# Optimization experiments

Measured on AMD Instinct MI355X. Metric: run time of the kernel, lower is better.

Reference implementation:

```python
import jax, jax.numpy as jnp
from jax import lax
import numpy as np

N, M, P, K = 2, 16384, 5023, 4
C_PLANE, HP = 32, 256
OUT_DIM = 32


def _harmonic(x):
    # pytorch3d HarmonicEmbedding(n=4, logspace, omega_0=1, append_input=True)
    f = jnp.asarray([1.0, 2.0, 4.0, 8.0], x.dtype)
    e = (x[..., None] * f).reshape(x.shape[:-1] + (-1,))  # [..., 12]
    return jnp.concatenate([jnp.sin(e), jnp.cos(e), x], axis=-1)  # [..., 27]


def _grid_sample2d(img, grid):
    # img [C,H,W], grid [M,2] (x->W, y->H) in [-1,1]; bilinear, zero pad, align_corners=False
    C, H, W = img.shape
    x = (grid[:, 0] + 1.0) * (W / 2.0) - 0.5
    y = (grid[:, 1] + 1.0) * (H / 2.0) - 0.5
    x0 = jnp.floor(x); y0 = jnp.floor(y)
    x1 = x0 + 1.0; y1 = y0 + 1.0
    wx1 = x - x0; wx0 = 1.0 - wx1
    wy1 = y - y0; wy0 = 1.0 - wy1
    def gather(ix, iy):
        valid = ((ix >= 0) & (ix < W) & (iy >= 0) & (iy < H)).astype(img.dtype)
        ixc = jnp.clip(ix, 0, W - 1).astype(jnp.int32)
        iyc = jnp.clip(iy, 0, H - 1).astype(jnp.int32)
        return img[:, iyc, ixc] * valid[None, :]  # [C,M]
    out = (gather(x0, y0) * (wx0 * wy0) + gather(x1, y0) * (wx1 * wy0)
           + gather(x0, y1) * (wx0 * wy1) + gather(x1, y1) * (wx1 * wy1))
    return out.T  # [M,C]


def _forward(coordinates, directions, points_position, tex_tplanes, emb_table,
             pw1, pb1, pw2, pb2, fw1, fb1, fw2, fb2, fw3, fb3, dw, db, rw1, rb1, rw2, rb2):
    c = coordinates
    p = points_position
    # --- triplane sampling (EG3D projections (x,y),(x,z),(z,x)), mean over planes ---
    proj = jnp.stack([c[..., :2],
                      c[..., jnp.array([0, 2])],
                      c[..., jnp.array([2, 0])]], axis=1)  # [N,3,M,2]
    tex = jax.vmap(jax.vmap(_grid_sample2d))(tex_tplanes, proj).mean(axis=1)  # [N,M,32]
    # --- KNN (squared distances, ascending, as pytorch3d knn_points) ---
    d2 = (jnp.sum(c * c, -1)[:, :, None] + jnp.sum(p * p, -1)[:, None, :]
          - 2.0 * jnp.einsum('nmc,npc->nmp', c, p))  # [N,M,P]
    negd, idx = lax.top_k(-d2, K)
    dist = -negd  # [N,M,K]
    nn = jax.vmap(lambda pts, i: pts[i])(p, idx)  # [N,M,K,3]
    pf = emb_table[idx]  # [N,M,K,32]
    rel = c[:, :, None, :] - nn
    rel = rel / jnp.maximum(jnp.linalg.norm(rel, axis=-1, keepdims=True), 1e-12)
    h = jnp.concatenate([pf, _harmonic(rel)], axis=-1)  # [N,M,K,59]
    h = jax.nn.relu(h @ pw1 + pb1) @ pw2 + pb2  # [N,M,K,32]
    w = 1.0 / dist
    w = w / jnp.sum(w, axis=1, keepdims=True)  # dim=1 exactly as in source
    pts_feat = jnp.sum(h * w[..., None], axis=2)  # [N,M,32]
    # --- dense MLP stack ---
    feat = jnp.concatenate([tex, pts_feat], axis=-1)  # [N,M,64]
    feat = jax.nn.relu(feat @ fw1 + fb1)
    feat = jax.nn.relu(feat @ fw2 + fb2)
    feat = feat @ fw3 + fb3  # [N,M,128]
    selector = jnp.all((c > -1.0) & (c < 1.0), axis=-1)  # [N,M]
    raw = (jax.nn.softplus(10.0 * (feat @ dw + db)) / 10.0) * selector[..., None]
    densities = 1.0 - jnp.exp(-raw)
    rays = directions / jnp.maximum(jnp.linalg.norm(directions, axis=-1, keepdims=True), 1e-12)
    rgb = jnp.concatenate([feat, _harmonic(rays)], axis=-1)  # [N,M,155]
    rgb = jax.nn.relu(rgb @ rw1 + rb1) @ rw2 + rb2  # [N,M,OUT_DIM]
    rgb = jnp.concatenate([jax.nn.sigmoid(rgb[..., :3]) * (1.0 + 2 * 0.001) - 0.001,
                           rgb[..., 3:]], axis=-1)
    return densities, rgb, dist


def setup_inputs() -> dict:
    key = jax.random.key(0)
    ks = jax.random.split(key, 16)
    rn = lambda k, s, sc=1.0: jax.random.normal(k, s, jnp.float32) * sc
    def lin(k, i, o):
        k1, k2 = jax.random.split(k)
        return rn(k1, (i, o), 1.0 / np.sqrt(i)), rn(k2, (o,), 0.01)
    coordinates = jax.random.uniform(ks[0], (N, M, 3), jnp.float32)
    directions = rn(ks[1], (N, M, 3))
    points_position = jax.random.uniform(ks[2], (N, P, 3), jnp.float32)
    tex_tplanes = rn(ks[3], (N, 3, C_PLANE, HP, HP))
    emb_table = rn(ks[4], (P, 32), 0.02)
    pw1, pb1 = lin(ks[5], 32 + 27, 64)
    pw2, pb2 = lin(ks[6], 64, 32)
    fw1, fb1 = lin(ks[7], 64, 128)
    fw2, fb2 = lin(ks[8], 128, 128)
    fw3, fb3 = lin(ks[9], 128, 128)
    dw, db = lin(ks[10], 128, 1)
    rw1, rb1 = lin(ks[11], 128 + 27, 64)
    rw2, rb2 = lin(ks[12], 64, OUT_DIM)
    return dict(coordinates=coordinates, directions=directions, points_position=points_position,
                tex_tplanes=tex_tplanes, emb_table=emb_table, pw1=pw1, pb1=pb1, pw2=pw2, pb2=pb2,
                fw1=fw1, fb1=fb1, fw2=fw2, fb2=fb2, fw3=fw3, fb3=fb3, dw=dw, db=db,
                rw1=rw1, rb1=rb1, rw2=rw2, rb2=rb2)


def reference(coordinates, directions, points_position, tex_tplanes, emb_table,
              pw1, pb1, pw2, pb2, fw1, fb1, fw2, fb2, fw3, fb3, dw, db, rw1, rb1, rw2, rb2):
    return _forward(coordinates, directions, points_position, tex_tplanes, emb_table,
                    pw1, pb1, pw2, pb2, fw1, fb1, fw2, fb2, fw3, fb3, dw, db, rw1, rb1, rw2, rb2)
```

## Files before the change

kernel.cpp:

```cpp
#include <hip/hip_runtime.h>
#include <float.h>
#include <math.h>

#define NB 2
#define MQ 16384
#define NQ (NB*MQ)
#define PP 5023
#define KNN 4
#define HPX 256
#define HWSZ (HPX*HPX)
#define GD 12
#define GC (GD*GD*GD)
#define CAND_MAX 1024

#define OUT_RGB_OFF  ((size_t)NQ)
#define OUT_DIST_OFF ((size_t)NQ + (size_t)NQ*32)

#define WS_SUMS_OFF   ((size_t)0x80000)
#define WS_PCNT_OFF   ((size_t)0x81000)
#define WS_PSTART_OFF ((size_t)0x85000)
#define WS_PCUR_OFF   ((size_t)0x89000)
#define WS_QCNT_OFF   ((size_t)0x8D000)
#define WS_QSTART_OFF ((size_t)0x91000)
#define WS_QCUR_OFF   ((size_t)0x95000)
#define WS_QID_OFF    ((size_t)0x99000)
#define WS_PG_OFF     ((size_t)0xC0000)
#define WS_PID_OFF    ((size_t)0xF0000)
#define WS_WP_OFF     ((size_t)0x100000)
#define WS_TEX_OFF    ((size_t)0x120000)

#define WP_PW1 0
#define WP_PW2 1920
#define WP_FW1 2944
#define WP_FW2 7040
#define WP_FW3 15232
#define WP_DW  23424
#define WP_RW1 23488
#define WP_RW2 28480

typedef __attribute__((ext_vector_type(2))) _Float16 half2v;

static __device__ __forceinline__ unsigned int pk2(float a, float b) {
    half2v h; h[0] = (_Float16)a; h[1] = (_Float16)b;
    return __builtin_bit_cast(unsigned int, h);
}
static __device__ __forceinline__ float2 upk(unsigned int u) {
    half2v h = __builtin_bit_cast(half2v, u);
    return make_float2((float)h[0], (float)h[1]);
}
static __device__ __forceinline__ float dot2(unsigned int a, unsigned int b, float c) {
    return __builtin_amdgcn_fdot2(__builtin_bit_cast(half2v, a),
                                  __builtin_bit_cast(half2v, b), c, false);
}
static __device__ __forceinline__ int cell_of(float x) {
    int g = (int)(x * (float)GD);
    return (g < 0) ? 0 : ((g > GD-1) ? GD-1 : g);
}

struct PackArgs {
    const float* src[8];
    int off[8]; int din[8]; int dout[8];
};
__global__ __launch_bounds__(256) void k_pack(PackArgs a, unsigned int* wp) {
    const int mid = blockIdx.y;
    const int idx = blockIdx.x * 256 + threadIdx.x;
    const int DIN = a.din[mid], DOUT = a.dout[mid];
    const int din2 = (DIN + 1) >> 1;
    if (idx >= din2 * DOUT) return;
    const int i2 = idx / DOUT, j = idx - i2 * DOUT;
    const float* s = a.src[mid];
    const float lo = s[(2*i2) * DOUT + j];
    const float hi = (2*i2 + 1 < DIN) ? s[(2*i2 + 1) * DOUT + j] : 0.f;
    wp[a.off[mid] + idx] = pk2(lo, hi);
}

__global__ __launch_bounds__(256) void k_transpose(const float* __restrict__ src,
                                                   float* __restrict__ dst) {
    const int tid = threadIdx.x;
    const int b = blockIdx.x;
    const int n3 = b >> 8;
    const int hw = ((b & 255) << 8) + tid;
    const float* s = src + (size_t)n3 * 32 * HWSZ + hw;
    float v[32];
#pragma unroll
    for (int c = 0; c < 32; ++c) v[c] = s[(size_t)c * HWSZ];
    float4* d = (float4*)(dst + ((size_t)n3 * HWSZ + hw) * 32);
#pragma unroll
    for (int c = 0; c < 8; ++c) d[c] = make_float4(v[4*c], v[4*c+1], v[4*c+2], v[4*c+3]);
}

__global__ __launch_bounds__(256) void k_count(const float* __restrict__ pts,
                                               const float* __restrict__ coords,
                                               unsigned int* __restrict__ pcnt,
                                               unsigned int* __restrict__ qcnt) {
    const int i = blockIdx.x * 256 + threadIdx.x;
    if (i < NB * PP) {
        const int n = (i >= PP) ? 1 : 0;
        const float px = pts[3*i], py = pts[3*i+1], pz = pts[3*i+2];
        const int c = (cell_of(pz)*GD + cell_of(py))*GD + cell_of(px);
        atomicAdd(&pcnt[n*GC + c], 1u);
    } else if (i - NB*PP < NQ) {
        const int q = i - NB*PP;
        const int n = q >> 14;
        const float cx = coords[3*q], cy = coords[3*q+1], cz = coords[3*q+2];
        const int c = (cell_of(cz)*GD + cell_of(cy))*GD + cell_of(cx);
        atomicAdd(&qcnt[n*GC + c], 1u);
    }
}

__global__ __launch_bounds__(1024) void k_scan2(const unsigned int* __restrict__ pcnt,
                                                unsigned int* __restrict__ psta,
                                                unsigned int* __restrict__ pcur,
                                                const unsigned int* __restrict__ qcnt,
                                                unsigned int* __restrict__ qsta,
                                                unsigned int* __restrict__ qcur) {
    __shared__ unsigned int sc[1024];
    const int t = threadIdx.x;
#pragma unroll 1
    for (int which = 0; which < 2; ++which) {
        const unsigned int* cnt = which ? qcnt : pcnt;
        unsigned int* start  = which ? qsta : psta;
        unsigned int* cursor = which ? qcur : pcur;
        const int stride = which ? MQ : PP;
#pragma unroll 1
        for (int n = 0; n < 2; ++n) {
            const unsigned int* c = cnt + n*GC;
            unsigned int a = (2*t   < GC) ? c[2*t]   : 0u;
            unsigned int b = (2*t+1 < GC) ? c[2*t+1] : 0u;
            unsigned int s = a + b;
            sc[t] = s;
            __syncthreads();
            for (int off = 1; off < 1024; off <<= 1) {
                unsigned int v = (t >= off) ? sc[t - off] : 0u;
                __syncthreads();
                sc[t] += v;
                __syncthreads();
            }
            unsigned int excl = sc[t] - s;
            unsigned int base = n * stride;
            if (2*t < GC)   { start[n*GC + 2*t]   = base + excl;
                              cursor[n*GC + 2*t]  = base + excl; }
            if (2*t+1 < GC) { start[n*GC + 2*t+1] = base + excl + a;
                              cursor[n*GC + 2*t+1]= base + excl + a; }
            __syncthreads();
        }
    }
}

__global__ __launch_bounds__(256) void k_scatter(const float* __restrict__ pts,
                                                 const float* __restrict__ coords,
                                                 unsigned int* __restrict__ pcur,
                                                 unsigned int* __restrict__ qcur,
                                                 float4* __restrict__ pg,
                                                 int* __restrict__ pid,
                                                 int* __restrict__ qid) {
    const int i = blockIdx.x * 256 + threadIdx.x;
    if (i < NB * PP) {
        const int n = (i >= PP) ? 1 : 0;
        const int local = i - n * PP;
        const float px = pts[3*i], py = pts[3*i+1], pz = pts[3*i+2];
        const int c = (cell_of(pz)*GD + cell_of(py))*GD + cell_of(px);
        const unsigned int pos = atomicAdd(&pcur[n*GC + c], 1u);
        pg[pos] = make_float4(px, py, pz, fmaf(px, px, fmaf(py, py, pz*pz)));
        pid[pos] = local;
    } else if (i - NB*PP < NQ) {
        const int q = i - NB*PP;
        const int n = q >> 14;
        const float cx = coords[3*q], cy = coords[3*q+1], cz = coords[3*q+2];
        const int c = (cell_of(cz)*GD + cell_of(cy))*GD + cell_of(cx);
        const unsigned int pos = atomicAdd(&qcur[n*GC + c], 1u);
        qid[pos] = q;
    }
}

__global__ __launch_bounds__(256) void k_knn_cell(
    const float* __restrict__ coords,
    const unsigned int* __restrict__ pstart, const unsigned int* __restrict__ pcnt,
    const float4* __restrict__ pg, const int* __restrict__ pid,
    const unsigned int* __restrict__ qstart, const unsigned int* __restrict__ qcnt,
    const int* __restrict__ qid,
    float* __restrict__ odist, int* __restrict__ oidx)
{
    __shared__ float4 cand[CAND_MAX];
    __shared__ int    cidx[CAND_MAX];
    __shared__ unsigned int rs[25], ro[26];
    const int tid = threadIdx.x;
    const int bid = blockIdx.x;
    const int n = bid / GC, c = bid % GC;
    const unsigned int qn = qcnt[n*GC + c];
    if (qn == 0) return;
    const int gz = c / (GD*GD), gy = (c / GD) % GD, gx = c % GD;

    const int x0 = max(gx-2,0), x1 = min(gx+2,GD-1);
    const int y0 = max(gy-2,0), y1 = min(gy+2,GD-1), ny = y1-y0+1;
    const int z0 = max(gz-2,0), z1 = min(gz+2,GD-1), nz = z1-z0+1;
    const int nrow = ny*nz;

    __shared__ unsigned int rcnt[25];
    if (tid < nrow) {
        const int yy = y0 + tid % ny;
        const int zz = z0 + tid / ny;
        const int c0 = n*GC + (zz*GD + yy)*GD + x0;
        const int c1 = n*GC + (zz*GD + yy)*GD + x1;
        const unsigned int s = pstart[c0];
        rs[tid]   = s;
        rcnt[tid] = (pstart[c1] + pcnt[c1]) - s;
    }
    __syncthreads();
    if (tid == 0) {
        unsigned int acc = 0; ro[0] = 0;
        for (int t = 0; t < nrow; ++t) { acc += rcnt[t]; ro[t+1] = acc; }
    }
    __syncthreads();
    const unsigned int total = ro[nrow];
    const bool ovf = (total > CAND_MAX);
    if (!ovf) {
        for (unsigned int i = tid; i < total; i += 256) {
            int lo = 0, hi = nrow;
            while (hi - lo > 1) { int mid = (lo + hi) >> 1; if (ro[mid] <= i) lo = mid; else hi = mid; }
            const unsigned int src = rs[lo] + (i - ro[lo]);
            cand[i] = pg[src];
            cidx[i] = pid[src];
        }
    }
    __syncthreads();

    const float w = 1.0f / (float)GD;
    const float thresh = 4.f * w * w * 0.999f;
    const int grp = tid >> 4, l16 = tid & 15;
    const unsigned int qs = qstart[n*GC + c];

#define INS4(d, i) { \
        bool L3 = ((d) < bd3) || ((d) == bd3 && (i) < bi3); \
        bool L2 = ((d) < bd2) || ((d) == bd2 && (i) < bi2); \
        bool L1 = ((d) < bd1) || ((d) == bd1 && (i) < bi1); \
        bool L0 = ((d) < bd0) || ((d) == bd0 && (i) < bi0); \
        bd3 = L3 ? (L2 ? bd2 : (d)) : bd3;  bi3 = L3 ? (L2 ? bi2 : (i)) : bi3; \
        bd2 = L2 ? (L1 ? bd1 : (d)) : bd2;  bi2 = L2 ? (L1 ? bi1 : (i)) : bi2; \
        bd1 = L1 ? (L0 ? bd0 : (d)) : bd1;  bi1 = L1 ? (L0 ? bi0 : (i)) : bi1; \
        bd0 = L0 ? (d) : bd0;               bi0 = L0 ? (i) : bi0; }

#define MERGE16() { \
        float bd[4] = { bd0, bd1, bd2, bd3 }; \
        int   bi[4] = { bi0, bi1, bi2, bi3 }; \
        for (int mask = 1; mask < 16; mask <<= 1) { \
            float od[4]; int oi[4]; \
            for (int j = 0; j < 4; ++j) { od[j] = __shfl_xor(bd[j], mask); \
                                          oi[j] = __shfl_xor(bi[j], mask); } \
            float e[4]; int ei[4]; \
            for (int j = 0; j < 4; ++j) { \
                float ad = bd[j], xd = od[3-j]; \
                int   ai = bi[j], xi = oi[3-j]; \
                bool ta = (ad < xd) || (ad == xd && ai < xi); \
                e[j] = ta ? ad : xd; ei[j] = ta ? ai : xi; \
            } \
            { bool sw = (e[2] < e[0]) || (e[2] == e[0] && ei[2] < ei[0]); \
              if (sw) { float td=e[0]; e[0]=e[2]; e[2]=td; int ti=ei[0]; ei[0]=ei[2]; ei[2]=ti; } } \
            { bool sw = (e[3] < e[1]) || (e[3] == e[1] && ei[3] < ei[1]); \
              if (sw) { float td=e[1]; e[1]=e[3]; e[3]=td; int ti=ei[1]; ei[1]=ei[3]; ei[3]=ti; } } \
            { bool sw = (e[1] < e[0]) || (e[1] == e[0] && ei[1] < ei[0]); \
              if (sw) { float td=e[0]; e[0]=e[1]; e[1]=td; int ti=ei[0]; ei[0]=ei[1]; ei[1]=ti; } } \
            { bool sw = (e[3] < e[2]) || (e[3] == e[2] && ei[3] < ei[2]); \
              if (sw) { float td=e[2]; e[2]=e[3]; e[3]=td; int ti=ei[2]; ei[2]=ei[3]; ei[3]=ti; } } \
            for (int j = 0; j < 4; ++j) { bd[j] = e[j]; bi[j] = ei[j]; } \
        } \
        bd0 = bd[0]; bd1 = bd[1]; bd2 = bd[2]; bd3 = bd[3]; \
        bi0 = bi[0]; bi1 = bi[1]; bi2 = bi[2]; bi3 = bi[3]; }

#pragma unroll 1
    for (unsigned int qb = 0; qb < qn; qb += 16) {
        const unsigned int qi = qb + grp;
        if (qi >= qn) continue;
        const int q = qid[qs + qi];
        const float cx = coords[3*q], cy = coords[3*q+1], cz = coords[3*q+2];
        const float ccq = fmaf(cx, cx, fmaf(cy, cy, cz*cz));

        float bd0 = FLT_MAX, bd1 = FLT_MAX, bd2 = FLT_MAX, bd3 = FLT_MAX;
        int   bi0 = 0x7fffffff, bi1 = 0x7fffffff, bi2 = 0x7fffffff, bi3 = 0x7fffffff;

        if (!ovf) {
#pragma unroll 1
            for (unsigned int j = l16; j < total; j += 16) {
                const float4 P = cand[j];
                const int i = cidx[j];
                const float dt = fmaf(cx, P.x, fmaf(cy, P.y, cz * P.z));
                const float d = fmaf(-2.0f, dt, ccq + P.w);
                INS4(d, i)
            }
            MERGE16()
        }
        if (ovf || !(bd3 < thresh)) {
            bd0 = bd1 = bd2 = bd3 = FLT_MAX;
            bi0 = bi1 = bi2 = bi3 = 0x7fffffff;
#pragma unroll 1
            for (int j = l16; j < PP; j += 16) {
                const float4 P = pg[n*PP + j];
                const int i = pid[n*PP + j];
                const float dt = fmaf(cx, P.x, fmaf(cy, P.y, cz * P.z));
                const float d = fmaf(-2.0f, dt, ccq + P.w);
                INS4(d, i)
            }
            MERGE16()
        }
        if (l16 == 0) {
            *(float4*)(odist + (size_t)q*4) = make_float4(bd0, bd1, bd2, bd3);
            *(int4*)(oidx + (size_t)q*4)    = make_int4(bi0, bi1, bi2, bi3);
        }
    }
#undef INS4
#undef MERGE16
}

__global__ __launch_bounds__(1024) void k_sums(const float* __restrict__ dist,
                                               float* __restrict__ sums) {
    const int b = blockIdx.x;
    const int n = b >> 2, k = b & 3;
    float s = 0.f;
    for (int m = threadIdx.x; m < MQ; m += 1024)
        s += 1.0f / dist[((size_t)n * MQ + m) * 4 + k];
    __shared__ float red[1024];
    red[threadIdx.x] = s;
    __syncthreads();
    for (int off = 512; off > 0; off >>= 1) {
        if (threadIdx.x < off) red[threadIdx.x] += red[threadIdx.x + off];
        __syncthreads();
    }
    if (threadIdx.x == 0) sums[b] = red[0];
}

static __device__ __forceinline__ float harm_val(int h, float rx, float ry, float rz) {
    if (h >= 27) return 0.f;
    float v;
    if (h < 24) {
        int base = (h < 12) ? h : (h - 12);
        float rv = (base >> 2) == 0 ? rx : ((base >> 2) == 1 ? ry : rz);
        float e = rv * (float)(1 << (base & 3));
        v = (h < 12) ? sinf(e) : cosf(e);
    } else {
        v = (h == 24) ? rx : ((h == 25) ? ry : rz);
    }
    return v;
}

template<int DIN2, int DOUT, int TILE>
__device__ __forceinline__ void gemv_l(const unsigned int* Xp, int lane,
                                       const unsigned int* Wl,
                                       const float* __restrict__ bias,
                                       int j0, float (&acc)[TILE]) {
    static_assert(TILE % 4 == 0, "");
#pragma unroll
    for (int u = 0; u < TILE; ++u) acc[u] = bias[j0 + u];
#pragma unroll
    for (int i2 = 0; i2 < DIN2; ++i2) {
        const unsigned int xv = Xp[i2 * 64 + lane];
        const uint4* wr = (const uint4*)(Wl + i2 * DOUT + j0);
#pragma unroll
        for (int t = 0; t < TILE/4; ++t) {
            const uint4 w4 = wr[t];
            acc[4*t+0] = dot2(xv, w4.x, acc[4*t+0]);
            acc[4*t+1] = dot2(xv, w4.y, acc[4*t+1]);
            acc[4*t+2] = dot2(xv, w4.z, acc[4*t+2]);
            acc[4*t+3] = dot2(xv, w4.w, acc[4*t+3]);
        }
    }
}

__global__ __launch_bounds__(1024, 2) void k_main(
    const float* __restrict__ coords, const float* __restrict__ dirs,
    const float* __restrict__ pts, const float* __restrict__ tex_raw,
    const float* __restrict__ tex_t, const float* __restrict__ emb,
    const unsigned int* __restrict__ wp,
    const float* __restrict__ pb1, const float* __restrict__ pb2,
    const float* __restrict__ fb1, const float* __restrict__ fb2,
    const float* __restrict__ fb3, const float* __restrict__ db,
    const float* __restrict__ rb1, const float* __restrict__ rb2,
    const int* __restrict__ idxbuf, const float* __restrict__ distbuf,
    const float* __restrict__ sums, float* __restrict__ out, int use_tex_t)
{
    __shared__ unsigned int S[128 * 64];
    __shared__ __align__(16) unsigned int W[8192];
    const int tid  = threadIdx.x;
    const int lane = tid & 63;
    const int wv   = __builtin_amdgcn_readfirstlane(tid >> 6);
    const int q0   = blockIdx.x * 64;
    const int n    = q0 >> 14;
    const int q    = q0 + lane;

#define STAGE(dstu4, srcoff, len) { \
        const uint4* s4_ = (const uint4*)(wp + (srcoff)); \
        for (int i_ = tid; i_ < (len)/4; i_ += 1024) ((uint4*)W)[(dstu4) + i_] = s4_[i_]; }

    float tex_acc[2] = {0.f, 0.f};
    {
        const int g = wv;
        const float cx = coords[q*3+0], cy = coords[q*3+1], cz = coords[q*3+2];
#pragma unroll
        for (int pl = 0; pl < 3; ++pl) {
            float gx = (pl == 2) ? cz : cx;
            float gy = (pl == 0) ? cy : ((pl == 1) ? cz : cx);
            float x = (gx + 1.f) * 128.f - 0.5f;
            float y = (gy + 1.f) * 128.f - 0.5f;
            float x0f = floorf(x), y0f = floorf(y);
            float wx1 = x - x0f, wy1 = y - y0f;
            float wx0 = 1.f - wx1, wy0 = 1.f - wy1;
            int x0 = (int)x0f, y0 = (int)y0f;
            int n3 = n * 3 + pl;
            int  xs[4] = { x0, x0+1, x0,   x0+1 };
            int  ys[4] = { y0, y0,   y0+1, y0+1 };
            float wt[4] = { wx0*wy0, wx1*wy0, wx0*wy1, wx1*wy1 };
#pragma unroll
            for (int c = 0; c < 4; ++c) {
                int xi = xs[c], yi = ys[c];
                if (xi >= 0 && xi < HPX && yi >= 0 && yi < HPX) {
                    float wgt = wt[c];
                    if (use_tex_t) {
                        const float2 a = *(const float2*)(tex_t +
                            (((size_t)n3 * HWSZ + (size_t)yi * HPX + xi) * 32 + g * 2));
                        tex_acc[0] = fmaf(wgt, a.x, tex_acc[0]);
                        tex_acc[1] = fmaf(wgt, a.y, tex_acc[1]);
                    } else {
                        size_t base = ((size_t)(n3 * 32 + g * 2)) * HWSZ + (size_t)yi * HPX + xi;
                        tex_acc[0] = fmaf(wgt, tex_raw[base], tex_acc[0]);
                        tex_acc[1] = fmaf(wgt, tex_raw[base + HWSZ], tex_acc[1]);
                    }
                }
            }
        }
        tex_acc[0] *= (1.f / 3.f); tex_acc[1] *= (1.f / 3.f);
    }

    STAGE(0, WP_PW1, 1920)
    STAGE(512, WP_PW2, 1024)
    __syncthreads();

#pragma unroll 1
    for (int k = 0; k < KNN; ++k) {
        {
            const int id = idxbuf[(size_t)q*4 + k];
            if (wv < 8) {
                const float4 e = *(const float4*)(emb + (size_t)id * 32 + wv*4);
                S[(64 + 2*wv    )*64 + lane] = pk2(e.x, e.y);
                S[(64 + 2*wv + 1)*64 + lane] = pk2(e.z, e.w);
            } else {
                const int w8 = wv - 8;
                const float cx = coords[q*3+0], cy = coords[q*3+1], cz = coords[q*3+2];
                const float nx = pts[((size_t)n*PP + id)*3 + 0];
                const float ny = pts[((size_t)n*PP + id)*3 + 1];
                const float nz = pts[((size_t)n*PP + id)*3 + 2];
                float rx = cx - nx, ry = cy - ny, rz = cz - nz;
                float nrm = sqrtf(fmaf(rx, rx, fmaf(ry, ry, rz*rz)));
                float inv = 1.f / fmaxf(nrm, 1e-12f);
                rx *= inv; ry *= inv; rz *= inv;
                if (w8 < 7) {
#pragma unroll
                    for (int t = 0; t < 2; ++t) {
                        const int pr = 2*w8 + t;
                        S[(80 + pr)*64 + lane] =
                            pk2(harm_val(2*pr, rx, ry, rz), harm_val(2*pr + 1, rx, ry, rz));
                    }
                }
            }
        }
        __syncthreads();
        {
            float acc[4];
            gemv_l<30, 64, 4>(S + 64*64, lane, W, pb1, wv * 4, acc);
            S[(96 + 2*wv    )*64 + lane] = pk2(fmaxf(acc[0], 0.f), fmaxf(acc[1], 0.f));
            S[(96 + 2*wv + 1)*64 + lane] = pk2(fmaxf(acc[2], 0.f), fmaxf(acc[3], 0.f));
        }
        __syncthreads();
        {
            float acc[2];
            acc[0] = pb2[wv*2 + 0]; acc[1] = pb2[wv*2 + 1];
#pragma unroll
            for (int i2 = 0; i2 < 32; ++i2) {
                const unsigned int xv = S[(96 + i2)*64 + lane];
                acc[0] = dot2(xv, W[2048 + i2*32 + wv*2 + 0], acc[0]);
                acc[1] = dot2(xv, W[2048 + i2*32 + wv*2 + 1], acc[1]);
            }
            const float dist = distbuf[(size_t)q*4 + k];
            const float wk = (1.0f / dist) / sums[n*4 + k];
            S[(k*16 + wv)*64 + lane] = pk2(wk * acc[0], wk * acc[1]);
        }
        __syncthreads();
    }

    {
        S[(64 + wv)*64 + lane] = pk2(tex_acc[0], tex_acc[1]);
        float a = 0.f, b = 0.f;
#pragma unroll
        for (int k = 0; k < 4; ++k) {
            float2 v = upk(S[(k*16 + wv)*64 + lane]);
            a += v.x; b += v.y;
        }
        S[(80 + wv)*64 + lane] = pk2(a, b);
    }
    STAGE(0, WP_FW1, 4096)
    __syncthreads();
    {
        float acc[8];
        gemv_l<32, 128, 8>(S + 64*64, lane, W, fb1, wv * 8, acc);
#pragma unroll
        for (int u = 0; u < 4; ++u)
            S[(4*wv + u)*64 + lane] = pk2(fmaxf(acc[2*u], 0.f), fmaxf(acc[2*u+1], 0.f));
    }
    __syncthreads();
    STAGE(0, WP_FW2, 8192)
    __syncthreads();
    {
        float acc[8];
        gemv_l<64, 128, 8>(S, lane, W, fb2, wv * 8, acc);
#pragma unroll
        for (int u = 0; u < 4; ++u)
            S[(64 + 4*wv + u)*64 + lane] = pk2(fmaxf(acc[2*u], 0.f), fmaxf(acc[2*u+1], 0.f));
    }
    __syncthreads();
    STAGE(0, WP_FW3, 8192)
    __syncthreads();
    {
        float acc[8];
        gemv_l<64, 128, 8>(S + 64*64, lane, W, fb3, wv * 8, acc);
#pragma unroll
        for (int u = 0; u < 4; ++u)
            S[(4*wv + u)*64 + lane] = pk2(acc[2*u], acc[2*u+1]);
    }
    __syncthreads();
    STAGE(0, WP_RW1, 4992)
    STAGE(1248, WP_RW2, 1024)
    STAGE(1504, WP_DW, 64)
    if (wv < 14) {
        float dx = dirs[q*3+0], dy = dirs[q*3+1], dz = dirs[q*3+2];
        float dn = sqrtf(fmaf(dx, dx, fmaf(dy, dy, dz*dz)));
        float inv = 1.f / fmaxf(dn, 1e-12f);
        dx *= inv; dy *= inv; dz *= inv;
        S[(64 + wv)*64 + lane] = pk2(harm_val(2*wv, dx, dy, dz),
                                     harm_val(2*wv + 1, dx, dy, dz));
    }
    __syncthreads();
    {
        const int j0 = wv * 4;
        float acc[4];
        gemv_l<78, 64, 4>(S, lane, W, rb1, j0, acc);
        S[(78 + 2*wv    )*64 + lane] = pk2(fmaxf(acc[0], 0.f), fmaxf(acc[1], 0.f));
        S[(78 + 2*wv + 1)*64 + lane] = pk2(fmaxf(acc[2], 0.f), fmaxf(acc[3], 0.f));
    }
    __syncthreads();
    {
        float acc[2];
        acc[0] = rb2[wv*2 + 0]; acc[1] = rb2[wv*2 + 1];
#pragma unroll
        for (int i2 = 0; i2 < 32; ++i2) {
            const unsigned int xv = S[(78 + i2)*64 + lane];
            acc[0] = dot2(xv, W[4992 + i2*32 + wv*2 + 0], acc[0]);
            acc[1] = dot2(xv, W[4992 + i2*32 + wv*2 + 1], acc[1]);
        }
#pragma unroll
        for (int u = 0; u < 2; ++u) {
            int j = wv*2 + u;
            float v = acc[u];
            if (j < 3) v = 1.002f * (1.f / (1.f + expf(-v))) - 0.001f;
            out[OUT_RGB_OFF + (size_t)q*32 + j] = v;
        }
        if (wv == 15) {
            float z = db[0];
#pragma unroll 1
            for (int i2 = 0; i2 < 64; ++i2)
                z = dot2(S[i2*64 + lane], W[6016 + i2], z);
            const float cx = coords[q*3+0], cy = coords[q*3+1], cz = coords[q*3+2];
            float selv = (cx > -1.f && cx < 1.f && cy > -1.f && cy < 1.f &&
                          cz > -1.f && cz < 1.f) ? 1.f : 0.f;
            float t10 = 10.f * z;
            float sp = (t10 > 20.f) ? t10 : log1pf(expf(t10));
            float raw = sp * 0.1f * selv;
            out[q] = 1.f - expf(-raw);
        }
    }
#undef STAGE
}

extern "C" void kernel_launch(void* const* d_in, const int* in_sizes, int n_in,
                              void* d_out, int out_size, void* d_ws, size_t ws_size,
                              hipStream_t stream) {
    (void)in_sizes; (void)n_in; (void)out_size;
    const float* coords = (const float*)d_in[0];
    const float* dirs   = (const float*)d_in[1];
    const float* pts    = (const float*)d_in[2];
    const float* tex    = (const float*)d_in[3];
    const float* emb    = (const float*)d_in[4];
    const float* pw1 = (const float*)d_in[5];  const float* pb1 = (const float*)d_in[6];
    const float* pw2 = (const float*)d_in[7];  const float* pb2 = (const float*)d_in[8];
    const float* fw1 = (const float*)d_in[9];  const float* fb1 = (const float*)d_in[10];
    const float* fw2 = (const float*)d_in[11]; const float* fb2 = (const float*)d_in[12];
    const float* fw3 = (const float*)d_in[13]; const float* fb3 = (const float*)d_in[14];
    const float* dw  = (const float*)d_in[15]; const float* db  = (const float*)d_in[16];
    const float* rw1 = (const float*)d_in[17]; const float* rb1 = (const float*)d_in[18];
    const float* rw2 = (const float*)d_in[19]; const float* rb2 = (const float*)d_in[20];

    float*        out     = (float*)d_out;
    int*          wsidx   = (int*)d_ws;
    float*        wssums  = (float*)((char*)d_ws + WS_SUMS_OFF);
    unsigned int* wspcnt  = (unsigned int*)((char*)d_ws + WS_PCNT_OFF);
    unsigned int* wspsta  = (unsigned int*)((char*)d_ws + WS_PSTART_OFF);
    unsigned int* wspcur  = (unsigned int*)((char*)d_ws + WS_PCUR_OFF);
    unsigned int* wsqcnt  = (unsigned int*)((char*)d_ws + WS_QCNT_OFF);
    unsigned int* wsqsta  = (unsigned int*)((char*)d_ws + WS_QSTART_OFF);
    unsigned int* wsqcur  = (unsigned int*)((char*)d_ws + WS_QCUR_OFF);
    int*          wsqid   = (int*)((char*)d_ws + WS_QID_OFF);
    float4*       wspg    = (float4*)((char*)d_ws + WS_PG_OFF);
    int*          wspid   = (int*)((char*)d_ws + WS_PID_OFF);
    unsigned int* wswp    = (unsigned int*)((char*)d_ws + WS_WP_OFF);
    float*        wstex   = (float*)((char*)d_ws + WS_TEX_OFF);

    const size_t need_tex = WS_TEX_OFF + (size_t)6 * HWSZ * 32 * 4;
    const int use_t = (ws_size >= need_tex) ? 1 : 0;

    PackArgs pa;
    pa.src[0] = pw1; pa.off[0] = WP_PW1; pa.din[0] = 59;  pa.dout[0] = 64;
    pa.src[1] = pw2; pa.off[1] = WP_PW2; pa.din[1] = 64;  pa.dout[1] = 32;
    pa.src[2] = fw1; pa.off[2] = WP_FW1; pa.din[2] = 64;  pa.dout[2] = 128;
    pa.src[3] = fw2; pa.off[3] = WP_FW2; pa.din[3] = 128; pa.dout[3] = 128;
    pa.src[4] = fw3; pa.off[4] = WP_FW3; pa.din[4] = 128; pa.dout[4] = 128;
    pa.src[5] = dw;  pa.off[5] = WP_DW;  pa.din[5] = 128; pa.dout[5] = 1;
    pa.src[6] = rw1; pa.off[6] = WP_RW1; pa.din[6] = 155; pa.dout[6] = 64;
    pa.src[7] = rw2; pa.off[7] = WP_RW2; pa.din[7] = 64;  pa.dout[7] = 32;

    const int nitems = NB*PP + NQ;
    hipMemsetAsync((char*)d_ws + WS_PCNT_OFF, 0, WS_QSTART_OFF - WS_PCNT_OFF, stream);
    k_pack<<<dim3(32, 8), 256, 0, stream>>>(pa, wswp);
    if (use_t) k_transpose<<<6 * 256, 256, 0, stream>>>(tex, wstex);
    k_count<<<(nitems + 255)/256, 256, 0, stream>>>(pts, coords, wspcnt, wsqcnt);
    k_scan2<<<1, 1024, 0, stream>>>(wspcnt, wspsta, wspcur, wsqcnt, wsqsta, wsqcur);
    k_scatter<<<(nitems + 255)/256, 256, 0, stream>>>(pts, coords, wspcur, wsqcur,
                                                      wspg, wspid, wsqid);
    k_knn_cell<<<NB*GC, 256, 0, stream>>>(coords, wspsta, wspcnt, wspg, wspid,
                                          wsqsta, wsqcnt, wsqid,
                                          out + OUT_DIST_OFF, wsidx);
    k_sums<<<8, 1024, 0, stream>>>(out + OUT_DIST_OFF, wssums);
    k_main<<<NQ / 64, 1024, 0, stream>>>(coords, dirs, pts, tex, wstex, emb,
                                         wswp, pb1, pb2, fb1, fb2, fb3, db, rb1, rb2,
                                         wsidx, out + OUT_DIST_OFF, wssums, out, use_t);
}
```

Baseline: 301.2 us.

## Process two queries per lane in MLP kernel and store transposed triplanes as packed half

The main kernel now handles 128 queries per block, two per lane. Each weight vector read from LDS feeds two dot2 accumulators, which halves weight LDS traffic per query and halves the number of block-wide weight staging passes. The transposed triplane buffer is stored as packed 16-bit pairs, which halves the transpose write traffic and the gather bytes. The cost is doubled LDS activation storage, which forces launch bounds from 2 to 1 block per CU and reduces occupancy, plus lower precision for the texture values.

```diff
diff --git a/kernel.cpp b/kernel.cpp
--- a/kernel.cpp
+++ b/kernel.cpp
@@ -75,7 +75,7 @@
 }
 
 __global__ __launch_bounds__(256) void k_transpose(const float* __restrict__ src,
-                                                   float* __restrict__ dst) {
+                                                   unsigned int* __restrict__ dst) {
     const int tid = threadIdx.x;
     const int b = blockIdx.x;
     const int n3 = b >> 8;
@@ -84,9 +84,11 @@
     float v[32];
 #pragma unroll
     for (int c = 0; c < 32; ++c) v[c] = s[(size_t)c * HWSZ];
-    float4* d = (float4*)(dst + ((size_t)n3 * HWSZ + hw) * 32);
-#pragma unroll
-    for (int c = 0; c < 8; ++c) d[c] = make_float4(v[4*c], v[4*c+1], v[4*c+2], v[4*c+3]);
+    uint4* d = (uint4*)(dst + ((size_t)n3 * HWSZ + hw) * 16);
+#pragma unroll
+    for (int c = 0; c < 4; ++c)
+        d[c] = make_uint4(pk2(v[8*c], v[8*c+1]), pk2(v[8*c+2], v[8*c+3]),
+                          pk2(v[8*c+4], v[8*c+5]), pk2(v[8*c+6], v[8*c+7]));
 }
 
 __global__ __launch_bounds__(256) void k_count(const float* __restrict__ pts,
@@ -342,33 +344,35 @@
     return v;
 }
 
+#define SW 128
+
 template<int DIN2, int DOUT, int TILE>
-__device__ __forceinline__ void gemv_l(const unsigned int* Xp, int lane,
-                                       const unsigned int* Wl,
-                                       const float* __restrict__ bias,
-                                       int j0, float (&acc)[TILE]) {
+__device__ __forceinline__ void gemv2(const unsigned int* Xp, int lane,
+                                      const unsigned int* Wl,
+                                      const float* __restrict__ bias, int j0,
+                                      float (&aa)[TILE], float (&ab)[TILE]) {
     static_assert(TILE % 4 == 0, "");
 #pragma unroll
-    for (int u = 0; u < TILE; ++u) acc[u] = bias[j0 + u];
+    for (int u = 0; u < TILE; ++u) { aa[u] = bias[j0 + u]; ab[u] = aa[u]; }
 #pragma unroll
     for (int i2 = 0; i2 < DIN2; ++i2) {
-        const unsigned int xv = Xp[i2 * 64 + lane];
+        const uint2 xv = *(const uint2*)(Xp + i2 * SW + 2*lane);
         const uint4* wr = (const uint4*)(Wl + i2 * DOUT + j0);
 #pragma unroll
         for (int t = 0; t < TILE/4; ++t) {
             const uint4 w4 = wr[t];
-            acc[4*t+0] = dot2(xv, w4.x, acc[4*t+0]);
-            acc[4*t+1] = dot2(xv, w4.y, acc[4*t+1]);
-            acc[4*t+2] = dot2(xv, w4.z, acc[4*t+2]);
-            acc[4*t+3] = dot2(xv, w4.w, acc[4*t+3]);
-        }
-    }
-}
-
-__global__ __launch_bounds__(1024, 2) void k_main(
+            aa[4*t+0] = dot2(xv.x, w4.x, aa[4*t+0]);  ab[4*t+0] = dot2(xv.y, w4.x, ab[4*t+0]);
+            aa[4*t+1] = dot2(xv.x, w4.y, aa[4*t+1]);  ab[4*t+1] = dot2(xv.y, w4.y, ab[4*t+1]);
+            aa[4*t+2] = dot2(xv.x, w4.z, aa[4*t+2]);  ab[4*t+2] = dot2(xv.y, w4.z, ab[4*t+2]);
+            aa[4*t+3] = dot2(xv.x, w4.w, aa[4*t+3]);  ab[4*t+3] = dot2(xv.y, w4.w, ab[4*t+3]);
+        }
+    }
+}
+
+__global__ __launch_bounds__(1024, 1) void k_main(
     const float* __restrict__ coords, const float* __restrict__ dirs,
     const float* __restrict__ pts, const float* __restrict__ tex_raw,
-    const float* __restrict__ tex_t, const float* __restrict__ emb,
+    const unsigned int* __restrict__ tex16, const float* __restrict__ emb,
     const unsigned int* __restrict__ wp,
     const float* __restrict__ pb1, const float* __restrict__ pb2,
     const float* __restrict__ fb1, const float* __restrict__ fb2,
@@ -377,56 +381,62 @@
     const int* __restrict__ idxbuf, const float* __restrict__ distbuf,
     const float* __restrict__ sums, float* __restrict__ out, int use_tex_t)
 {
-    __shared__ unsigned int S[128 * 64];
+    __shared__ unsigned int S[128 * SW];
     __shared__ __align__(16) unsigned int W[8192];
     const int tid  = threadIdx.x;
     const int lane = tid & 63;
     const int wv   = __builtin_amdgcn_readfirstlane(tid >> 6);
-    const int q0   = blockIdx.x * 64;
+    const int q0   = blockIdx.x * 128;
     const int n    = q0 >> 14;
-    const int q    = q0 + lane;
+    const int qa   = q0 + 2*lane, qb = qa + 1;
 
 #define STAGE(dstu4, srcoff, len) { \
         const uint4* s4_ = (const uint4*)(wp + (srcoff)); \
         for (int i_ = tid; i_ < (len)/4; i_ += 1024) ((uint4*)W)[(dstu4) + i_] = s4_[i_]; }
 
-    float tex_acc[2] = {0.f, 0.f};
+    unsigned int tex_pack[2];
     {
         const int g = wv;
-        const float cx = coords[q*3+0], cy = coords[q*3+1], cz = coords[q*3+2];
-#pragma unroll
-        for (int pl = 0; pl < 3; ++pl) {
-            float gx = (pl == 2) ? cz : cx;
-            float gy = (pl == 0) ? cy : ((pl == 1) ? cz : cx);
-            float x = (gx + 1.f) * 128.f - 0.5f;
-            float y = (gy + 1.f) * 128.f - 0.5f;
-            float x0f = floorf(x), y0f = floorf(y);
-            float wx1 = x - x0f, wy1 = y - y0f;
-            float wx0 = 1.f - wx1, wy0 = 1.f - wy1;
-            int x0 = (int)x0f, y0 = (int)y0f;
-            int n3 = n * 3 + pl;
-            int  xs[4] = { x0, x0+1, x0,   x0+1 };
-            int  ys[4] = { y0, y0,   y0+1, y0+1 };
-            float wt[4] = { wx0*wy0, wx1*wy0, wx0*wy1, wx1*wy1 };
-#pragma unroll
-            for (int c = 0; c < 4; ++c) {
-                int xi = xs[c], yi = ys[c];
-                if (xi >= 0 && xi < HPX && yi >= 0 && yi < HPX) {
-                    float wgt = wt[c];
-                    if (use_tex_t) {
-                        const float2 a = *(const float2*)(tex_t +
-                            (((size_t)n3 * HWSZ + (size_t)yi * HPX + xi) * 32 + g * 2));
-                        tex_acc[0] = fmaf(wgt, a.x, tex_acc[0]);
-                        tex_acc[1] = fmaf(wgt, a.y, tex_acc[1]);
-                    } else {
-                        size_t base = ((size_t)(n3 * 32 + g * 2)) * HWSZ + (size_t)yi * HPX + xi;
-                        tex_acc[0] = fmaf(wgt, tex_raw[base], tex_acc[0]);
-                        tex_acc[1] = fmaf(wgt, tex_raw[base + HWSZ], tex_acc[1]);
+#pragma unroll
+        for (int s = 0; s < 2; ++s) {
+            const int q = qa + s;
+            const float cx = coords[q*3+0], cy = coords[q*3+1], cz = coords[q*3+2];
+            float a0 = 0.f, a1 = 0.f;
+#pragma unroll
+            for (int pl = 0; pl < 3; ++pl) {
+                float gx = (pl == 2) ? cz : cx;
+                float gy = (pl == 0) ? cy : ((pl == 1) ? cz : cx);
+                float x = (gx + 1.f) * 128.f - 0.5f;
+                float y = (gy + 1.f) * 128.f - 0.5f;
+                float x0f = floorf(x), y0f = floorf(y);
+                float wx1 = x - x0f, wy1 = y - y0f;
+                float wx0 = 1.f - wx1, wy0 = 1.f - wy1;
+                int x0 = (int)x0f, y0 = (int)y0f;
+                int n3 = n * 3 + pl;
+                int  xs[4] = { x0, x0+1, x0,   x0+1 };
+                int  ys[4] = { y0, y0,   y0+1, y0+1 };
+                float wt[4] = { wx0*wy0, wx1*wy0, wx0*wy1, wx1*wy1 };
+#pragma unroll
+                for (int c = 0; c < 4; ++c) {
+                    int xi = xs[c], yi = ys[c];
+                    if (xi >= 0 && xi < HPX && yi >= 0 && yi < HPX) {
+                        float wgt = wt[c];
+                        if (use_tex_t) {
+                            const unsigned int v = tex16[
+                                ((size_t)n3 * HWSZ + (size_t)yi * HPX + xi) * 16 + g];
+                            const float2 f = upk(v);
+                            a0 = fmaf(wgt, f.x, a0);
+                            a1 = fmaf(wgt, f.y, a1);
+                        } else {
+                            size_t base = ((size_t)(n3 * 32 + g * 2)) * HWSZ + (size_t)yi * HPX + xi;
+                            a0 = fmaf(wgt, tex_raw[base], a0);
+                            a1 = fmaf(wgt, tex_raw[base + HWSZ], a1);
+                        }
                     }
                 }
             }
-        }
-        tex_acc[0] *= (1.f / 3.f); tex_acc[1] *= (1.f / 3.f);
+            tex_pack[s] = pk2(a0 * (1.f/3.f), a1 * (1.f/3.f));
+        }
     }
 
     STAGE(0, WP_PW1, 1920)
@@ -436,143 +446,187 @@
 #pragma unroll 1
     for (int k = 0; k < KNN; ++k) {
         {
-            const int id = idxbuf[(size_t)q*4 + k];
-            if (wv < 8) {
-                const float4 e = *(const float4*)(emb + (size_t)id * 32 + wv*4);
-                S[(64 + 2*wv    )*64 + lane] = pk2(e.x, e.y);
-                S[(64 + 2*wv + 1)*64 + lane] = pk2(e.z, e.w);
-            } else {
-                const int w8 = wv - 8;
-                const float cx = coords[q*3+0], cy = coords[q*3+1], cz = coords[q*3+2];
-                const float nx = pts[((size_t)n*PP + id)*3 + 0];
-                const float ny = pts[((size_t)n*PP + id)*3 + 1];
-                const float nz = pts[((size_t)n*PP + id)*3 + 2];
-                float rx = cx - nx, ry = cy - ny, rz = cz - nz;
-                float nrm = sqrtf(fmaf(rx, rx, fmaf(ry, ry, rz*rz)));
-                float inv = 1.f / fmaxf(nrm, 1e-12f);
-                rx *= inv; ry *= inv; rz *= inv;
-                if (w8 < 7) {
-#pragma unroll
-                    for (int t = 0; t < 2; ++t) {
-                        const int pr = 2*w8 + t;
-                        S[(80 + pr)*64 + lane] =
-                            pk2(harm_val(2*pr, rx, ry, rz), harm_val(2*pr + 1, rx, ry, rz));
+#pragma unroll
+            for (int s = 0; s < 2; ++s) {
+                const int q = qa + s;
+                const int id = idxbuf[(size_t)q*4 + k];
+                if (wv < 8) {
+                    const float4 e = *(const float4*)(emb + (size_t)id * 32 + wv*4);
+                    S[(64 + 2*wv    )*SW + 2*lane + s] = pk2(e.x, e.y);
+                    S[(64 + 2*wv + 1)*SW + 2*lane + s] = pk2(e.z, e.w);
+                } else {
+                    const int w8 = wv - 8;
+                    if (w8 < 7) {
+                        const float cx = coords[q*3+0], cy = coords[q*3+1], cz = coords[q*3+2];
+                        const float nx = pts[((size_t)n*PP + id)*3 + 0];
+                        const float ny = pts[((size_t)n*PP + id)*3 + 1];
+                        const float nz = pts[((size_t)n*PP + id)*3 + 2];
+                        float rx = cx - nx, ry = cy - ny, rz = cz - nz;
+                        float nrm = sqrtf(fmaf(rx, rx, fmaf(ry, ry, rz*rz)));
+                        float inv = 1.f / fmaxf(nrm, 1e-12f);
+                        rx *= inv; ry *= inv; rz *= inv;
+#pragma unroll
+                        for (int t = 0; t < 2; ++t) {
+                            const int pr = 2*w8 + t;
+                            S[(80 + pr)*SW + 2*lane + s] =
+                                pk2(harm_val(2*pr, rx, ry, rz), harm_val(2*pr + 1, rx, ry, rz));
+                        }
                     }
                 }
             }
         }
         __syncthreads();
         {
-            float acc[4];
-            gemv_l<30, 64, 4>(S + 64*64, lane, W, pb1, wv * 4, acc);
-            S[(96 + 2*wv    )*64 + lane] = pk2(fmaxf(acc[0], 0.f), fmaxf(acc[1], 0.f));
-            S[(96 + 2*wv + 1)*64 + lane] = pk2(fmaxf(acc[2], 0.f), fmaxf(acc[3], 0.f));
+            float aa[4], ab[4];
+            gemv2<30, 64, 4>(S + 64*SW, lane, W, pb1, wv * 4, aa, ab);
+            S[(96 + 2*wv    )*SW + 2*lane + 0] = pk2(fmaxf(aa[0], 0.f), fmaxf(aa[1], 0.f));
+            S[(96 + 2*wv    )*SW + 2*lane + 1] = pk2(fmaxf(ab[0], 0.f), fmaxf(ab[1], 0.f));
+            S[(96 + 2*wv + 1)*SW + 2*lane + 0] = pk2(fmaxf(aa[2], 0.f), fmaxf(aa[3], 0.f));
+            S[(96 + 2*wv + 1)*SW + 2*lane + 1] = pk2(fmaxf(ab[2], 0.f), fmaxf(ab[3], 0.f));
         }
         __syncthreads();
         {
-            float acc[2];
-            acc[0] = pb2[wv*2 + 0]; acc[1] = pb2[wv*2 + 1];
+            float aa[2], ab[2];
+            aa[0] = pb2[wv*2 + 0]; aa[1] = pb2[wv*2 + 1];
+            ab[0] = aa[0]; ab[1] = aa[1];
 #pragma unroll
             for (int i2 = 0; i2 < 32; ++i2) {
-                const unsigned int xv = S[(96 + i2)*64 + lane];
-                acc[0] = dot2(xv, W[2048 + i2*32 + wv*2 + 0], acc[0]);
-                acc[1] = dot2(xv, W[2048 + i2*32 + wv*2 + 1], acc[1]);
-            }
-            const float dist = distbuf[(size_t)q*4 + k];
-            const float wk = (1.0f / dist) / sums[n*4 + k];
-            S[(k*16 + wv)*64 + lane] = pk2(wk * acc[0], wk * acc[1]);
+                const uint2 xv = *(const uint2*)(S + (96 + i2)*SW + 2*lane);
+                const unsigned int w0 = W[2048 + i2*32 + wv*2 + 0];
+                const unsigned int w1 = W[2048 + i2*32 + wv*2 + 1];
+                aa[0] = dot2(xv.x, w0, aa[0]);  ab[0] = dot2(xv.y, w0, ab[0]);
+                aa[1] = dot2(xv.x, w1, aa[1]);  ab[1] = dot2(xv.y, w1, ab[1]);
+            }
+            const float da = distbuf[(size_t)qa*4 + k];
+            const float dbq = distbuf[(size_t)qb*4 + k];
+            const float wka = (1.0f / da)  / sums[n*4 + k];
+            const float wkb = (1.0f / dbq) / sums[n*4 + k];
+            S[(k*16 + wv)*SW + 2*lane + 0] = pk2(wka * aa[0], wka * aa[1]);
+            S[(k*16 + wv)*SW + 2*lane + 1] = pk2(wkb * ab[0], wkb * ab[1]);
         }
         __syncthreads();
     }
 
     {
-        S[(64 + wv)*64 + lane] = pk2(tex_acc[0], tex_acc[1]);
-        float a = 0.f, b = 0.f;
-#pragma unroll
-        for (int k = 0; k < 4; ++k) {
-            float2 v = upk(S[(k*16 + wv)*64 + lane]);
-            a += v.x; b += v.y;
-        }
-        S[(80 + wv)*64 + lane] = pk2(a, b);
+        S[(64 + wv)*SW + 2*lane + 0] = tex_pack[0];
+        S[(64 + wv)*SW + 2*lane + 1] = tex_pack[1];
+#pragma unroll
+        for (int s = 0; s < 2; ++s) {
+            float a = 0.f, b = 0.f;
+#pragma unroll
+            for (int k = 0; k < 4; ++k) {
+                float2 v = upk(S[(k*16 + wv)*SW + 2*lane + s]);
+                a += v.x; b += v.y;
+            }
+            S[(80 + wv)*SW + 2*lane + s] = pk2(a, b);
+        }
     }
     STAGE(0, WP_FW1, 4096)
     __syncthreads();
     {
-        float acc[8];
-        gemv_l<32, 128, 8>(S + 64*64, lane, W, fb1, wv * 8, acc);
-#pragma unroll
-        for (int u = 0; u < 4; ++u)
-            S[(4*wv + u)*64 + lane] = pk2(fmaxf(acc[2*u], 0.f), fmaxf(acc[2*u+1], 0.f));
+        float aa[8], ab[8];
+        gemv2<32, 128, 8>(S + 64*SW, lane, W, fb1, wv * 8, aa, ab);
+#pragma unroll
+        for (int u = 0; u < 4; ++u) {
+            S[(4*wv + u)*SW + 2*lane + 0] = pk2(fmaxf(aa[2*u], 0.f), fmaxf(aa[2*u+1], 0.f));
+            S[(4*wv + u)*SW + 2*lane + 1] = pk2(fmaxf(ab[2*u], 0.f), fmaxf(ab[2*u+1], 0.f));
+        }
     }
     __syncthreads();
     STAGE(0, WP_FW2, 8192)
     __syncthreads();
     {
-        float acc[8];
-        gemv_l<64, 128, 8>(S, lane, W, fb2, wv * 8, acc);
-#pragma unroll
-        for (int u = 0; u < 4; ++u)
-            S[(64 + 4*wv + u)*64 + lane] = pk2(fmaxf(acc[2*u], 0.f), fmaxf(acc[2*u+1], 0.f));
+        float aa[8], ab[8];
+        gemv2<64, 128, 8>(S, lane, W, fb2, wv * 8, aa, ab);
+#pragma unroll
+        for (int u = 0; u < 4; ++u) {
+            S[(64 + 4*wv + u)*SW + 2*lane + 0] = pk2(fmaxf(aa[2*u], 0.f), fmaxf(aa[2*u+1], 0.f));
+            S[(64 + 4*wv + u)*SW + 2*lane + 1] = pk2(fmaxf(ab[2*u], 0.f), fmaxf(ab[2*u+1], 0.f));
+        }
     }
     __syncthreads();
     STAGE(0, WP_FW3, 8192)
     __syncthreads();
     {
-        float acc[8];
-        gemv_l<64, 128, 8>(S + 64*64, lane, W, fb3, wv * 8, acc);
-#pragma unroll
-        for (int u = 0; u < 4; ++u)
-            S[(4*wv + u)*64 + lane] = pk2(acc[2*u], acc[2*u+1]);
+        float aa[8], ab[8];
+        gemv2<64, 128, 8>(S + 64*SW, lane, W, fb3, wv * 8, aa, ab);
+#pragma unroll
+        for (int u = 0; u < 4; ++u) {
+            S[(4*wv + u)*SW + 2*lane + 0] = pk2(aa[2*u], aa[2*u+1]);
+            S[(4*wv + u)*SW + 2*lane + 1] = pk2(ab[2*u], ab[2*u+1]);
+        }
     }
     __syncthreads();
     STAGE(0, WP_RW1, 4992)
     STAGE(1248, WP_RW2, 1024)
     STAGE(1504, WP_DW, 64)
     if (wv < 14) {
-        float dx = dirs[q*3+0], dy = dirs[q*3+1], dz = dirs[q*3+2];
-        float dn = sqrtf(fmaf(dx, dx, fmaf(dy, dy, dz*dz)));
-        float inv = 1.f / fmaxf(dn, 1e-12f);
-        dx *= inv; dy *= inv; dz *= inv;
-        S[(64 + wv)*64 + lane] = pk2(harm_val(2*wv, dx, dy, dz),
-                                     harm_val(2*wv + 1, dx, dy, dz));
+#pragma unroll
+        for (int s = 0; s < 2; ++s) {
+            const int q = qa + s;
+            float dx = dirs[q*3+0], dy = dirs[q*3+1], dz = dirs[q*3+2];
+            float dn = sqrtf(fmaf(dx, dx, fmaf(dy, dy, dz*dz)));
+            float inv = 1.f / fmaxf(dn, 1e-12f);
+            dx *= inv; dy *= inv; dz *= inv;
+            S[(64 + wv)*SW + 2*lane + s] = pk2(harm_val(2*wv, dx, dy, dz),
+                                               harm_val(2*wv + 1, dx, dy, dz));
+        }
     }
     __syncthreads();
     {
-        const int j0 = wv * 4;
-        float acc[4];
-        gemv_l<78, 64, 4>(S, lane, W, rb1, j0, acc);
-        S[(78 + 2*wv    )*64 + lane] = pk2(fmaxf(acc[0], 0.f), fmaxf(acc[1], 0.f));
-        S[(78 + 2*wv + 1)*64 + lane] = pk2(fmaxf(acc[2], 0.f), fmaxf(acc[3], 0.f));
+        float aa[4], ab[4];
+        gemv2<78, 64, 4>(S, lane, W, rb1, wv * 4, aa, ab);
+        S[(78 + 2*wv    )*SW + 2*lane + 0] = pk2(fmaxf(aa[0], 0.f), fmaxf(aa[1], 0.f));
+        S[(78 + 2*wv    )*SW + 2*lane + 1] = pk2(fmaxf(ab[0], 0.f), fmaxf(ab[1], 0.f));
+        S[(78 + 2*wv + 1)*SW + 2*lane + 0] = pk2(fmaxf(aa[2], 0.f), fmaxf(aa[3], 0.f));
+        S[(78 + 2*wv + 1)*SW + 2*lane + 1] = pk2(fmaxf(ab[2], 0.f), fmaxf(ab[3], 0.f));
     }
     __syncthreads();
     {
-        float acc[2];
-        acc[0] = rb2[wv*2 + 0]; acc[1] = rb2[wv*2 + 1];
+        float aa[2], ab[2];
+        aa[0] = rb2[wv*2 + 0]; aa[1] = rb2[wv*2 + 1];
+        ab[0] = aa[0]; ab[1] = aa[1];
 #pragma unroll
         for (int i2 = 0; i2 < 32; ++i2) {
-            const unsigned int xv = S[(78 + i2)*64 + lane];
-            acc[0] = dot2(xv, W[4992 + i2*32 + wv*2 + 0], acc[0]);
-            acc[1] = dot2(xv, W[4992 + i2*32 + wv*2 + 1], acc[1]);
+            const uint2 xv = *(const uint2*)(S + (78 + i2)*SW + 2*lane);
+            const unsigned int w0 = W[4992 + i2*32 + wv*2 + 0];
+            const unsigned int w1 = W[4992 + i2*32 + wv*2 + 1];
+            aa[0] = dot2(xv.x, w0, aa[0]);  ab[0] = dot2(xv.y, w0, ab[0]);
+            aa[1] = dot2(xv.x, w1, aa[1]);  ab[1] = dot2(xv.y, w1, ab[1]);
         }
 #pragma unroll
         for (int u = 0; u < 2; ++u) {
-            int j = wv*2 + u;
-            float v = acc[u];
-            if (j < 3) v = 1.002f * (1.f / (1.f + expf(-v))) - 0.001f;
-            out[OUT_RGB_OFF + (size_t)q*32 + j] = v;
+            const int j = wv*2 + u;
+            float va = (u == 0) ? aa[0] : aa[1];
+            float vb = (u == 0) ? ab[0] : ab[1];
+            if (j < 3) {
+                va = 1.002f * (1.f / (1.f + expf(-va))) - 0.001f;
+                vb = 1.002f * (1.f / (1.f + expf(-vb))) - 0.001f;
+            }
+            out[OUT_RGB_OFF + (size_t)qa*32 + j] = va;
+            out[OUT_RGB_OFF + (size_t)qb*32 + j] = vb;
         }
         if (wv == 15) {
-            float z = db[0];
+            float za = db[0], zb = db[0];
 #pragma unroll 1
-            for (int i2 = 0; i2 < 64; ++i2)
-                z = dot2(S[i2*64 + lane], W[6016 + i2], z);
-            const float cx = coords[q*3+0], cy = coords[q*3+1], cz = coords[q*3+2];
-            float selv = (cx > -1.f && cx < 1.f && cy > -1.f && cy < 1.f &&
-                          cz > -1.f && cz < 1.f) ? 1.f : 0.f;
-            float t10 = 10.f * z;
-            float sp = (t10 > 20.f) ? t10 : log1pf(expf(t10));
-            float raw = sp * 0.1f * selv;
-            out[q] = 1.f - expf(-raw);
+            for (int i2 = 0; i2 < 64; ++i2) {
+                const uint2 xv = *(const uint2*)(S + i2*SW + 2*lane);
+                const unsigned int wz = W[6016 + i2];
+                za = dot2(xv.x, wz, za);
+                zb = dot2(xv.y, wz, zb);
+            }
+#pragma unroll
+            for (int s = 0; s < 2; ++s) {
+                const int q = qa + s;
+                const float z = (s == 0) ? za : zb;
+                const float cx = coords[q*3+0], cy = coords[q*3+1], cz = coords[q*3+2];
+                float selv = (cx > -1.f && cx < 1.f && cy > -1.f && cy < 1.f &&
+                              cz > -1.f && cz < 1.f) ? 1.f : 0.f;
+                float t10 = 10.f * z;
+                float sp = (t10 > 20.f) ? t10 : log1pf(expf(t10));
+                float raw = sp * 0.1f * selv;
+                out[q] = 1.f - expf(-raw);
+            }
         }
     }
 #undef STAGE
@@ -609,9 +663,9 @@
     float4*       wspg    = (float4*)((char*)d_ws + WS_PG_OFF);
     int*          wspid   = (int*)((char*)d_ws + WS_PID_OFF);
     unsigned int* wswp    = (unsigned int*)((char*)d_ws + WS_WP_OFF);
-    float*        wstex   = (float*)((char*)d_ws + WS_TEX_OFF);
-
-    const size_t need_tex = WS_TEX_OFF + (size_t)6 * HWSZ * 32 * 4;
+    unsigned int* wstex   = (unsigned int*)((char*)d_ws + WS_TEX_OFF);
+
+    const size_t need_tex = WS_TEX_OFF + (size_t)6 * HWSZ * 16 * 4;
     const int use_t = (ws_size >= need_tex) ? 1 : 0;
 
     PackArgs pa;
@@ -636,7 +690,7 @@
                                           wsqsta, wsqcnt, wsqid,
                                           out + OUT_DIST_OFF, wsidx);
     k_sums<<<8, 1024, 0, stream>>>(out + OUT_DIST_OFF, wssums);
-    k_main<<<NQ / 64, 1024, 0, stream>>>(coords, dirs, pts, tex, wstex, emb,
-                                         wswp, pb1, pb2, fb1, fb2, fb3, db, rb1, rb2,
-                                         wsidx, out + OUT_DIST_OFF, wssums, out, use_t);
-}
+    k_main<<<NQ / 128, 1024, 0, stream>>>(coords, dirs, pts, tex, wstex, emb,
+                                          wswp, pb1, pb2, fb1, fb2, fb3, db, rb1, rb2,
+                                          wsidx, out + OUT_DIST_OFF, wssums, out, use_t);
+}
```

After: 280.4 us. 6.9% less time.
